# Kernel tuning notes

Hardware: AMD Instinct MI355X
Metric: run time of the kernel (lower is better)

The kernel has to match this reference:

```python
import jax, jax.numpy as jnp
import numpy as np


def setup_inputs() -> dict:
    key = jax.random.key(0)
    k1, k2 = jax.random.split(key)
    x = jax.random.normal(k1, (32, 128, 128, 128), dtype=jnp.float32)
    conv_w = jax.random.normal(k2, (1, 2, 7, 7), dtype=jnp.float32) * 0.1
    return {"x": x, "conv_w": conv_w}


def reference(x, conv_w):
    # x: [B, C, H, W]; conv_w: [1, 2, 7, 7]
    max_out = jnp.max(x, axis=1, keepdims=True)   # [B,1,H,W]
    avg_out = jnp.mean(x, axis=1, keepdims=True)  # [B,1,H,W]
    stacked = jnp.concatenate([avg_out, max_out], axis=1)  # [B,2,H,W]
    attn = jax.lax.conv_general_dilated(
        stacked, conv_w,
        window_strides=(1, 1), padding=((3, 3), (3, 3)),
        dimension_numbers=("NCHW", "OIHW", "NCHW"),
    )  # [B,1,H,W]
    return x * jax.nn.sigmoid(attn)
```

## Files before the change

kernel.cpp:

```cpp
#include <hip/hip_runtime.h>

#define BB 32
#define CC 128
#define HH 128
#define WW 128
#define HWSZ (HH * WW)
#define CHW (CC * HWSZ)
#define S4 (HWSZ / 4)
#define RPB 8
#define HALO 14

typedef float vfloat4 __attribute__((ext_vector_type(4)));

__device__ __forceinline__ vfloat4 fmax4(vfloat4 a, vfloat4 b) {
    vfloat4 r;
    r.x = fmaxf(a.x, b.x);
    r.y = fmaxf(a.y, b.y);
    r.z = fmaxf(a.z, b.z);
    r.w = fmaxf(a.w, b.w);
    return r;
}


__global__ __launch_bounds__(256) void k1_reduce(
    const float* __restrict__ x, float* __restrict__ maps) {
    const int tid = threadIdx.x;
    const int wg  = blockIdx.x;
    const int b   = wg >> 4;
    const int hb  = wg & 15;
    const int gh  = hb * RPB + (tid >> 5);
    const int w4  = tid & 31;

    const vfloat4* p = (const vfloat4*)(x + (size_t)b * CHW + gh * WW) + w4;
    vfloat4 v = p[0];
    vfloat4 sum = v, mx = v;
    #pragma unroll 8
    for (int c = 1; c < CC; ++c) {
        vfloat4 t = p[(size_t)c * S4];
        sum += t;
        mx = fmax4(mx, t);
    }
    vfloat4 avg = sum * (1.0f / (float)CC);
    *((vfloat4*)(maps + ((size_t)b * 2 + 0) * HWSZ + gh * WW) + w4) = avg;
    *((vfloat4*)(maps + ((size_t)b * 2 + 1) * HWSZ + gh * WW) + w4) = mx;
}

__global__ __launch_bounds__(256, 2) void k2_conv_mul(
    const float* __restrict__ x, const float* __restrict__ maps,
    const float* __restrict__ cw, float* __restrict__ out) {
    __shared__ float m_lds[2][HALO][WW];
    __shared__ float sig_lds[RPB][WW];
    __shared__ float wsh[2 * 49];

    const int tid = threadIdx.x;
    const int wg  = blockIdx.x;
    const int xcd = wg & 7;
    const int lin = wg >> 3;
    const int b   = xcd * 4 + (lin >> 4);
    const int hb  = lin & 15;
    const int h0  = hb * RPB;

    if (tid < 98) wsh[tid] = cw[tid];

    for (int i = tid; i < 2 * HALO * 32; i += 256) {
        const int ic = i / (HALO * 32);
        const int rem = i - ic * (HALO * 32);
        const int rr = rem >> 5;
        const int w4 = rem & 31;
        const int gh = h0 - 3 + rr;
        vfloat4 v = {0.f, 0.f, 0.f, 0.f};
        if (gh >= 0 && gh < HH)
            v = *((const vfloat4*)(maps + ((size_t)b * 2 + ic) * HWSZ + gh * WW) + w4);
        *(vfloat4*)&m_lds[ic][rr][w4 * 4] = v;
    }
    __syncthreads();

    {
        const int q = tid >> 7;
        const int w = tid & 127;
        float attn[4] = {0.f, 0.f, 0.f, 0.f};
        #pragma unroll
        for (int ic = 0; ic < 2; ++ic) {
            #pragma unroll
            for (int L = 0; L < 10; ++L) {
                const float* row = &m_lds[ic][q * 4 + L][0];
                #pragma unroll
                for (int kw = 0; kw < 7; ++kw) {
                    int wi = w - 3 + kw;
                    float v = (wi >= 0 && wi < WW) ? row[wi] : 0.0f;
                    #pragma unroll
                    for (int j = 0; j < 4; ++j) {
                        const int kh = L - j;
                        if (kh >= 0 && kh <= 6)
                            attn[j] = fmaf(v, wsh[ic * 49 + kh * 7 + kw], attn[j]);
                    }
                }
            }
        }
        #pragma unroll
        for (int j = 0; j < 4; ++j)
            sig_lds[q * 4 + j][w] = 1.0f / (1.0f + __expf(-attn[j]));
    }
    __syncthreads();

    {
        const float* xb = x + (size_t)b * CHW;
        const int wv = tid >> 6;
        const int ln = tid & 63;
        vfloat4 sgv[4];
        #pragma unroll
        for (int j = 0; j < 4; ++j) {
            int idx = ln + 64 * j;
            sgv[j] = *(const vfloat4*)&sig_lds[idx >> 5][(idx & 31) * 4];
        }
        const size_t slab_off = (size_t)h0 * WW;
        #pragma unroll 2
        for (int k = 31; k >= 0; --k) {
            const int c = wv + 4 * k;
            const vfloat4* ps = (const vfloat4*)(xb + (size_t)c * HWSZ + slab_off);
            vfloat4* po = (vfloat4*)(out + (size_t)b * CHW + (size_t)c * HWSZ + slab_off);
            vfloat4 v0 = ps[ln];
            vfloat4 v1 = ps[ln + 64];
            vfloat4 v2 = ps[ln + 128];
            vfloat4 v3 = ps[ln + 192];
            __builtin_nontemporal_store(v0 * sgv[0], po + ln);
            __builtin_nontemporal_store(v1 * sgv[1], po + ln + 64);
            __builtin_nontemporal_store(v2 * sgv[2], po + ln + 128);
            __builtin_nontemporal_store(v3 * sgv[3], po + ln + 192);
        }
    }
}

__global__ __launch_bounds__(256, 2) void sa_onepass(
    const float* __restrict__ x, const float* __restrict__ cw,
    float* __restrict__ out) {
    __shared__ float m_lds[2][HALO][WW];
    __shared__ float sig_lds[RPB][WW];
    __shared__ float wsh[2 * 49];

    const int tid = threadIdx.x;
    const int wg  = blockIdx.x;
    const int xcd = wg & 7;
    const int lin = wg >> 3;
    const int b   = xcd * 4 + (lin >> 4);
    const int hb  = lin & 15;
    const int h0  = hb * RPB;

    if (tid < 98) wsh[tid] = cw[tid];

    const int r0 = tid >> 5;
    const int w4 = tid & 31;
    const float* xb = x + (size_t)b * CHW;

    const bool actB = (r0 < HALO - 8);
    const int gh_a = h0 - 3 + r0;
    const int gh_b = h0 - 3 + r0 + 8;
    const bool okA = (gh_a >= 0) && (gh_a < HH);
    const bool okB = actB && (gh_b < HH);
    const int cha = gh_a < 0 ? 0 : (gh_a > HH - 1 ? HH - 1 : gh_a);
    const int chb = gh_b > HH - 1 ? HH - 1 : gh_b;

    const vfloat4* pA = (const vfloat4*)(xb + cha * WW) + w4;
    const vfloat4* pB = (const vfloat4*)(xb + chb * WW) + w4;

    vfloat4 sumA, mxA;
    {
        vfloat4 v = pA[0];
        sumA = v; mxA = v;
    }
    #pragma unroll 8
    for (int c = 1; c < CC; ++c) {
        vfloat4 v = pA[(size_t)c * S4];
        sumA += v;
        mxA = fmax4(mxA, v);
    }
    vfloat4 sumB = {0.f, 0.f, 0.f, 0.f}, mxB = sumB;
    if (actB) {
        vfloat4 v = pB[0];
        sumB = v; mxB = v;
        #pragma unroll 8
        for (int c = 1; c < CC; ++c) {
            vfloat4 t = pB[(size_t)c * S4];
            sumB += t;
            mxB = fmax4(mxB, t);
        }
    }

    const float invC = 1.0f / (float)CC;
    {
        vfloat4 avgA = sumA * invC;
        if (!okA) { avgA = (vfloat4){0,0,0,0}; mxA = (vfloat4){0,0,0,0}; }
        *(vfloat4*)&m_lds[0][r0][w4 * 4] = avgA;
        *(vfloat4*)&m_lds[1][r0][w4 * 4] = mxA;
        if (actB) {
            vfloat4 avgB = sumB * invC;
            if (!okB) { avgB = (vfloat4){0,0,0,0}; mxB = (vfloat4){0,0,0,0}; }
            *(vfloat4*)&m_lds[0][r0 + 8][w4 * 4] = avgB;
            *(vfloat4*)&m_lds[1][r0 + 8][w4 * 4] = mxB;
        }
    }
    __syncthreads();

    {
        const int q = tid >> 7;
        const int w = tid & 127;
        float attn[4] = {0.f, 0.f, 0.f, 0.f};
        #pragma unroll
        for (int ic = 0; ic < 2; ++ic) {
            #pragma unroll
            for (int L = 0; L < 10; ++L) {
                const float* row = &m_lds[ic][q * 4 + L][0];
                #pragma unroll
                for (int kw = 0; kw < 7; ++kw) {
                    int wi = w - 3 + kw;
                    float v = (wi >= 0 && wi < WW) ? row[wi] : 0.0f;
                    #pragma unroll
                    for (int j = 0; j < 4; ++j) {
                        const int kh = L - j;
                        if (kh >= 0 && kh <= 6)
                            attn[j] = fmaf(v, wsh[ic * 49 + kh * 7 + kw], attn[j]);
                    }
                }
            }
        }
        #pragma unroll
        for (int j = 0; j < 4; ++j)
            sig_lds[q * 4 + j][w] = 1.0f / (1.0f + __expf(-attn[j]));
    }
    __syncthreads();

    {
        const int wv = tid >> 6;
        const int ln = tid & 63;
        vfloat4 sgv[4];
        #pragma unroll
        for (int j = 0; j < 4; ++j) {
            int idx = ln + 64 * j;
            sgv[j] = *(const vfloat4*)&sig_lds[idx >> 5][(idx & 31) * 4];
        }
        const size_t slab_off = (size_t)h0 * WW;
        #pragma unroll 2
        for (int k = 31; k >= 0; --k) {
            const int c = wv + 4 * k;
            const vfloat4* ps = (const vfloat4*)(xb + (size_t)c * HWSZ + slab_off);
            vfloat4* po = (vfloat4*)(out + (size_t)b * CHW + (size_t)c * HWSZ + slab_off);
            vfloat4 v0 = ps[ln];
            vfloat4 v1 = ps[ln + 64];
            vfloat4 v2 = ps[ln + 128];
            vfloat4 v3 = ps[ln + 192];
            __builtin_nontemporal_store(v0 * sgv[0], po + ln);
            __builtin_nontemporal_store(v1 * sgv[1], po + ln + 64);
            __builtin_nontemporal_store(v2 * sgv[2], po + ln + 128);
            __builtin_nontemporal_store(v3 * sgv[3], po + ln + 192);
        }
    }
}

extern "C" void kernel_launch(void* const* d_in, const int* in_sizes, int n_in,
                              void* d_out, int out_size, void* d_ws, size_t ws_size,
                              hipStream_t stream) {
    const float* x  = (const float*)d_in[0];
    const float* cw = (const float*)d_in[1];
    float* out = (float*)d_out;

    const size_t maps_bytes = (size_t)BB * 2 * HWSZ * sizeof(float);
    if (ws_size >= maps_bytes) {
        float* maps = (float*)d_ws;
        k1_reduce<<<BB * (HH / RPB), 256, 0, stream>>>(x, maps);
        k2_conv_mul<<<BB * (HH / RPB), 256, 0, stream>>>(x, maps, cw, out);
    } else {
        sa_onepass<<<BB * (HH / RPB), 256, 0, stream>>>(x, cw, out);
    }
}
```

Measured before the change: 133.0 us.

## Fuse reduce and conv-multiply into a cooperative kernel holding x in registers

Replaces the two-kernel reduce-then-conv pipeline with one cooperative kernel of 256 blocks. Each block reads its 4-row band of x for 8 batches at a time, keeps the values in registers, writes the channel mean/max maps, does a grid-wide sync to get halo rows, then computes the 7x7 conv and sigmoid and scales the register-held x. This is meant to cut the second full read of x. In exchange it adds four grid syncs, needs 128 VGPRs for x per thread, and runs at limited occupancy.

```diff
diff --git a/kernel.cpp b/kernel.cpp
--- a/kernel.cpp
+++ b/kernel.cpp
@@ -1,4 +1,7 @@
 #include <hip/hip_runtime.h>
+#include <hip/hip_cooperative_groups.h>
+
+namespace cg = cooperative_groups;
 
 #define BB 32
 #define CC 128
@@ -7,8 +10,6 @@
 #define HWSZ (HH * WW)
 #define CHW (CC * HWSZ)
 #define S4 (HWSZ / 4)
-#define RPB 8
-#define HALO 14
 
 typedef float vfloat4 __attribute__((ext_vector_type(4)));
 
@@ -21,6 +22,117 @@
     return r;
 }
 
+__global__ __launch_bounds__(512, 2) void sa_coop(
+    const float* __restrict__ x, const float* __restrict__ cw,
+    float* __restrict__ out, float* __restrict__ maps) {
+    __shared__ float psum_s[4][4][WW];
+    __shared__ float psum_m[4][4][WW];
+    __shared__ float m_lds[2][10][WW];
+    __shared__ float sig_lds[4][WW];
+    __shared__ float wsh[2 * 49];
+
+    const int tid = threadIdx.x;
+    const int blk = blockIdx.x;
+    const int xcd = blk & 7;
+    const int lin = blk >> 3;
+    const int bq  = lin >> 2;
+    const int band = xcd * 4 + (lin & 3);
+    const int h0 = band * 4;
+
+    const int cgp = tid >> 7;
+    const int rp  = (tid >> 5) & 3;
+    const int w4p = tid & 31;
+
+    if (tid < 98) wsh[tid] = cw[tid];
+
+    cg::grid_group grid = cg::this_grid();
+
+    vfloat4 v[32];
+
+    for (int g = 0; g < 4; ++g) {
+        __syncthreads();
+        const int b = g * 8 + bq;
+        const float* xb = x + (size_t)b * CHW;
+
+        {
+            const float* base = xb + (size_t)(cgp * 32) * HWSZ + (h0 + rp) * WW;
+            vfloat4 s, m;
+            v[0] = *((const vfloat4*)base + w4p);
+            s = v[0]; m = v[0];
+            #pragma unroll
+            for (int i = 1; i < 32; ++i) {
+                v[i] = *((const vfloat4*)(base + (size_t)i * HWSZ) + w4p);
+                s += v[i];
+                m = fmax4(m, v[i]);
+            }
+            *(vfloat4*)&psum_s[cgp][rp][w4p * 4] = s;
+            *(vfloat4*)&psum_m[cgp][rp][w4p * 4] = m;
+        }
+        __syncthreads();
+        if (tid < 128) {
+            const int r = tid >> 5, w4 = tid & 31;
+            vfloat4 s = *(vfloat4*)&psum_s[0][r][w4 * 4];
+            vfloat4 m = *(vfloat4*)&psum_m[0][r][w4 * 4];
+            #pragma unroll
+            for (int c = 1; c < 4; ++c) {
+                s += *(vfloat4*)&psum_s[c][r][w4 * 4];
+                m = fmax4(m, *(vfloat4*)&psum_m[c][r][w4 * 4]);
+            }
+            vfloat4 avg = s * (1.0f / (float)CC);
+            *(vfloat4*)&m_lds[0][3 + r][w4 * 4] = avg;
+            *(vfloat4*)&m_lds[1][3 + r][w4 * 4] = m;
+            *((vfloat4*)(maps + ((size_t)b * 2 + 0) * HWSZ + (h0 + r) * WW) + w4) = avg;
+            *((vfloat4*)(maps + ((size_t)b * 2 + 1) * HWSZ + (h0 + r) * WW) + w4) = m;
+        }
+        __threadfence();
+        grid.sync();
+
+        if (tid < 384) {
+            const int ic = tid / 192;
+            const int rem = tid - ic * 192;
+            const int ridx = rem >> 5;
+            const int w4 = rem & 31;
+            const int rr = (ridx < 3) ? ridx : ridx + 4;
+            const int gh = h0 - 3 + rr;
+            vfloat4 val = {0.f, 0.f, 0.f, 0.f};
+            if (gh >= 0 && gh < HH)
+                val = *((const vfloat4*)(maps + ((size_t)b * 2 + ic) * HWSZ + gh * WW) + w4);
+            *(vfloat4*)&m_lds[ic][rr][w4 * 4] = val;
+        }
+        __syncthreads();
+        {
+            const int r = tid >> 7;
+            const int w = tid & 127;
+            float attn = 0.f;
+            #pragma unroll
+            for (int ic = 0; ic < 2; ++ic) {
+                #pragma unroll
+                for (int kh = 0; kh < 7; ++kh) {
+                    const float* row = &m_lds[ic][r + kh][0];
+                    #pragma unroll
+                    for (int kw = 0; kw < 7; ++kw) {
+                        int wi = w - 3 + kw;
+                        float vv = (wi >= 0 && wi < WW) ? row[wi] : 0.0f;
+                        attn = fmaf(vv, wsh[ic * 49 + kh * 7 + kw], attn);
+                    }
+                }
+            }
+            sig_lds[r][w] = 1.0f / (1.0f + __expf(-attn));
+        }
+        __syncthreads();
+
+        {
+            vfloat4 sg = *(const vfloat4*)&sig_lds[rp][w4p * 4];
+            float* ob = out + (size_t)b * CHW + (size_t)(cgp * 32) * HWSZ + (h0 + rp) * WW;
+            #pragma unroll
+            for (int i = 0; i < 32; ++i)
+                __builtin_nontemporal_store(v[i] * sg, (vfloat4*)(ob + (size_t)i * HWSZ) + w4p);
+        }
+    }
+}
+
+#define RPB 8
+#define HALO 14
 
 __global__ __launch_bounds__(256) void k1_reduce(
     const float* __restrict__ x, float* __restrict__ maps) {
@@ -266,8 +378,13 @@
     const size_t maps_bytes = (size_t)BB * 2 * HWSZ * sizeof(float);
     if (ws_size >= maps_bytes) {
         float* maps = (float*)d_ws;
-        k1_reduce<<<BB * (HH / RPB), 256, 0, stream>>>(x, maps);
-        k2_conv_mul<<<BB * (HH / RPB), 256, 0, stream>>>(x, maps, cw, out);
+        void* args[] = {(void*)&x, (void*)&cw, (void*)&out, (void*)&maps};
+        hipError_t e = hipLaunchCooperativeKernel((void*)sa_coop, dim3(256), dim3(512),
+                                                  args, 0, stream);
+        if (e != hipSuccess) {
+            k1_reduce<<<BB * (HH / RPB), 256, 0, stream>>>(x, maps);
+            k2_conv_mul<<<BB * (HH / RPB), 256, 0, stream>>>(x, maps, cw, out);
+        }
     } else {
         sa_onepass<<<BB * (HH / RPB), 256, 0, stream>>>(x, cw, out);
     }
```

Result: slower. 474.9 us (+257.1%).
